# Kernel tuning notes

Hardware: AMD Instinct MI355X
Metric: run time of the kernel (lower is better)

## Reference

```python
import jax, jax.numpy as jnp
import numpy as np

N = 8192
E = 262144
D = 512

def _glorot(key, shape):
    fan_in, fan_out = shape[0], shape[1]
    lim = np.sqrt(6.0 / (fan_in + fan_out)).astype(np.float32)
    return jax.random.uniform(key, shape, jnp.float32, -lim, lim)

def setup_inputs() -> dict:
    key = jax.random.key(0)
    ks = jax.random.split(key, 16)
    x = jax.random.normal(ks[0], (N, D), jnp.float32)
    edge_index = jax.random.randint(ks[1], (2, E), 0, N, jnp.int64)
    return {
        "x": x,
        "edge_index": edge_index,
        # SAGEConv: lin_l applied to aggregated neighbors (has bias), lin_r to root
        "W_l": _glorot(ks[2], (D, D)), "b_l": jnp.zeros((D,), jnp.float32),
        "W_r": _glorot(ks[3], (D, D)),
        "Wa": _glorot(ks[4], (D, 256)), "ba": jnp.zeros((256,), jnp.float32),
        "W1": _glorot(ks[5], (256, 128)), "b1": jnp.zeros((128,), jnp.float32),
        "W2": _glorot(ks[6], (128, 64)), "b2": jnp.zeros((64,), jnp.float32),
        "W3": _glorot(ks[7], (64, 3)), "b3": jnp.zeros((3,), jnp.float32),
    }

def _sage_mean(x, edge_index):
    # message from src -> dst, mean aggregation over incoming edges
    src, dst = edge_index[0], edge_index[1]
    msg_sum = jax.ops.segment_sum(x[src], dst, num_segments=N)  # [N, D]
    deg = jax.ops.segment_sum(jnp.ones((edge_index.shape[1],), x.dtype), dst, num_segments=N)
    return msg_sum / jnp.maximum(deg, 1.0)[:, None]

def _cdist(y):
    # pairwise euclidean distances, stable sqrt (0 on the diagonal)
    sq = jnp.sum(y * y, axis=-1)
    d2 = sq[:, None] + sq[None, :] - 2.0 * (y @ y.T)
    d2 = jnp.maximum(d2, 0.0)
    safe = jnp.where(d2 > 0.0, d2, 1.0)
    return jnp.where(d2 > 0.0, jnp.sqrt(safe), 0.0)

def reference(x, edge_index, W_l, b_l, W_r, Wa, ba, W1, b1, W2, b2, W3, b3):
    agg = _sage_mean(x, edge_index)
    h = agg @ W_l + b_l + x @ W_r          # SAGEConv output [N, 512]
    h = jax.nn.relu(h)
    h = jax.nn.relu(h @ Wa + ba)           # [N, 256]
    h = jax.nn.relu(h @ W1 + b1)           # [N, 128]
    h = jax.nn.relu(h @ W2 + b2)           # [N, 64]
    h = h @ W3 + b3                        # [N, 3]
    return _cdist(h)                       # [N, N]
```

## Files before the change

### kernel.cpp

```cpp
#include <hip/hip_runtime.h>
#include <math.h>

#define NN 8192
#define DD 512
#define HB 64
#define PAD 128

typedef _Float16 f16;
typedef _Float16 half8 __attribute__((ext_vector_type(8)));
typedef _Float16 half4 __attribute__((ext_vector_type(4)));
typedef float f32x4 __attribute__((ext_vector_type(4)));

typedef const __attribute__((address_space(1))) unsigned int* gptr_t;
typedef __attribute__((address_space(3))) unsigned int* lptr_t;

__device__ __forceinline__ void gload16(const void* g, void* l) {
    __builtin_amdgcn_global_load_lds((gptr_t)g, (lptr_t)l, 16, 0, 0);
}

__device__ __forceinline__ void transpose_tile(const float* __restrict__ W,
                                               f16* __restrict__ Wt,
                                               int Kw, int Nw, int bx, int by,
                                               float (*tile)[33]) {
    int n0 = bx * 32, k0 = by * 32;
    int t = threadIdx.x;
    {
        int r = t >> 3, cq = (t & 7) * 4;
        float4 v = *(const float4*)(W + (size_t)(k0 + r) * Nw + n0 + cq);
        tile[r][cq] = v.x; tile[r][cq + 1] = v.y; tile[r][cq + 2] = v.z; tile[r][cq + 3] = v.w;
    }
    __syncthreads();
    {
        int n = t >> 3, rq = (t & 7) * 4;
        half4 h;
        h[0] = (f16)tile[rq][n];     h[1] = (f16)tile[rq + 1][n];
        h[2] = (f16)tile[rq + 2][n]; h[3] = (f16)tile[rq + 3][n];
        *(half4*)(Wt + (size_t)(n0 + n) * Kw + k0 + rq) = h;
    }
}

__global__ __launch_bounds__(256) void prep_hist(const float* __restrict__ x,
                                                 f16* __restrict__ xh,
                                                 const float* __restrict__ W_l, f16* __restrict__ Wlt,
                                                 const float* __restrict__ W_r, f16* __restrict__ Wrt,
                                                 const float* __restrict__ Wa,  f16* __restrict__ Wat,
                                                 const float* __restrict__ W1,  f16* __restrict__ W1t,
                                                 const int* __restrict__ ei,
                                                 int* __restrict__ locoff, int E) {
    __shared__ float tile[32][33];
    __shared__ int h[NN];
    int b = blockIdx.x;
    int t = threadIdx.x;
    if (b < 4096) {
        int i = b * 256 + t;
        float4 v = ((const float4*)x)[i];
        half4 hh;
        hh[0] = (f16)v.x; hh[1] = (f16)v.y; hh[2] = (f16)v.z; hh[3] = (f16)v.w;
        ((half4*)xh)[i] = hh;
        return;
    }
    b -= 4096;
    if (b < 256)      { transpose_tile(W_l, Wlt, 512, 512, b & 15, b >> 4, tile); return; }
    b -= 256;
    if (b < 256)      { transpose_tile(W_r, Wrt, 512, 512, b & 15, b >> 4, tile); return; }
    b -= 256;
    if (b < 128)      { transpose_tile(Wa, Wat, 512, 256, b & 7, b >> 3, tile); return; }
    b -= 128;
    if (b < 32)       { transpose_tile(W1, W1t, 256, 128, b & 3, b >> 2, tile); return; }
    b -= 32;
#pragma unroll
    for (int i = 0; i < NN / 256; i++) h[i * 256 + t] = 0;
    __syncthreads();
    int epb = (E + HB - 1) / HB;
    int e0 = b * epb, e1 = min(e0 + epb, E);
    for (int e = e0 + t; e < e1; e += 256)
        atomicAdd(&h[ei[E + e]], 1);
    __syncthreads();
#pragma unroll
    for (int i = 0; i < NN / 256; i++) {
        int n = i * 256 + t;
        locoff[(size_t)b * NN + n] = h[n];
    }
}

__global__ __launch_bounds__(256) void offs_kernel(int* __restrict__ locoff,
                                                   int* __restrict__ deg) {
    int n = blockIdx.x * 256 + threadIdx.x;
    int s = 0;
#pragma unroll 8
    for (int b = 0; b < HB; b++) {
        int v = locoff[(size_t)b * NN + n];
        locoff[(size_t)b * NN + n] = s;
        s += v;
    }
    deg[n] = s;
}

__global__ __launch_bounds__(256) void scatter_kernel(const int* __restrict__ ei,
                                                      const int* __restrict__ locoff,
                                                      int* __restrict__ csr_pad, int E) {
    __shared__ int cur[NN];
    int b = blockIdx.x, t = threadIdx.x;
#pragma unroll
    for (int i = 0; i < NN / 256; i++) {
        int n = i * 256 + t;
        cur[n] = locoff[(size_t)b * NN + n];
    }
    __syncthreads();
    int epb = (E + HB - 1) / HB;
    int e0 = b * epb, e1 = min(e0 + epb, E);
    for (int e = e0 + t; e < e1; e += 256) {
        int dst = ei[E + e];
        int src = ei[e];
        int slot = atomicAdd(&cur[dst], 1);
        if (slot < PAD)
            csr_pad[((size_t)dst << 7) + slot] = src;
    }
}

__global__ __launch_bounds__(256) void agg_kernel(const f16* __restrict__ xh,
                                                  const int* __restrict__ deg,
                                                  const int* __restrict__ csr_pad,
                                                  f16* __restrict__ aggh) {
    int node = blockIdx.x * 4 + (threadIdx.x >> 6);
    int l = threadIdx.x & 63;
    int e = deg[node];
    if (e > PAD) e = PAD;
    const int* lst = csr_pad + (node << 7);
    const half8* xb = (const half8*)xh;
    float acc[8] = {0, 0, 0, 0, 0, 0, 0, 0};
    int p = 0;
    for (; p + 4 <= e; p += 4) {
        int s0 = lst[p], s1 = lst[p + 1], s2 = lst[p + 2], s3 = lst[p + 3];
        half8 v0 = xb[(size_t)s0 * 64 + l];
        half8 v1 = xb[(size_t)s1 * 64 + l];
        half8 v2 = xb[(size_t)s2 * 64 + l];
        half8 v3 = xb[(size_t)s3 * 64 + l];
#pragma unroll
        for (int j = 0; j < 8; j++)
            acc[j] += (float)v0[j] + (float)v1[j] + (float)v2[j] + (float)v3[j];
    }
    for (; p < e; p++) {
        half8 v = xb[(size_t)lst[p] * 64 + l];
#pragma unroll
        for (int j = 0; j < 8; j++) acc[j] += (float)v[j];
    }
    float inv = 1.0f / fmaxf((float)deg[node], 1.0f);
    half8 h;
#pragma unroll
    for (int j = 0; j < 8; j++) h[j] = (f16)(acc[j] * inv);
    ((half8*)aggh)[(size_t)node * 64 + l] = h;
}

template<int BN>
__global__ __launch_bounds__(256) void gemm_thin(const f16* __restrict__ A1,
                                                 const f16* __restrict__ B1,
                                                 const f16* __restrict__ A2,
                                                 const f16* __restrict__ B2,
                                                 const float* __restrict__ bias,
                                                 f16* __restrict__ C,
                                                 int N, int K, int relu) {
    constexpr int BM = 32;
    constexpr int FM = 2;
    constexpr int FN = BN / 64;
    constexpr int ACH = BM / 16;
    constexpr int NCH = (BM + BN) / 16;
    __shared__ f16 As[2][BM * 32];
    __shared__ f16 Bs[2][BN * 32];

    const int tid = threadIdx.x;
    const int l = tid & 63;
    const int wid = tid >> 6;
    const int row0 = blockIdx.y * BM;
    const int col0 = blockIdx.x * BN;
    const int rowc = l >> 2;
    const int sp = l & 3;

    f32x4 acc[FM][FN];
#pragma unroll
    for (int i = 0; i < FM; i++)
#pragma unroll
        for (int j = 0; j < FN; j++)
#pragma unroll
            for (int q = 0; q < 4; q++) acc[i][j][q] = 0.0f;

    const int ktiles = K >> 5;
    const int npass = (A2 != nullptr) ? 2 : 1;
    const int nt = ktiles * npass;

    auto stage = [&](int buf, int t) {
        int pass = (t >= ktiles) ? 1 : 0;
        int kk = (t - pass * ktiles) << 5;
        const f16* Ag = pass ? A2 : A1;
        const f16* Bg = pass ? B2 : B1;
#pragma unroll
        for (int c = wid; c < NCH; c += 4) {
            bool isA = (c < ACH);
            int cc = isA ? c : c - ACH;
            int row = cc * 16 + rowc;
            int slot = sp ^ ((row >> 1) & 3);
            const f16* g;
            f16* ld;
            if (isA) {
                g = Ag + (size_t)(row0 + row) * K + kk + slot * 8;
                ld = &As[buf][cc * 512];
            } else {
                g = Bg + (size_t)(col0 + row) * K + kk + slot * 8;
                ld = &Bs[buf][cc * 512];
            }
            gload16(g, ld);
        }
    };

    stage(0, 0);
    __syncthreads();
    for (int t = 0; t < nt; ++t) {
        int cur = t & 1;
        if (t + 1 < nt) stage(cur ^ 1, t + 1);
        half8 af[FM], bf[FN];
#pragma unroll
        for (int i = 0; i < FM; i++) {
            int r = i * 16 + (l & 15);
            int off = r * 64 + ((((l >> 4) ^ ((r >> 1) & 3))) << 4);
            af[i] = *(const half8*)((const char*)As[cur] + off);
        }
#pragma unroll
        for (int j = 0; j < FN; j++) {
            int r = wid * FN * 16 + j * 16 + (l & 15);
            int off = r * 64 + ((((l >> 4) ^ ((r >> 1) & 3))) << 4);
            bf[j] = *(const half8*)((const char*)Bs[cur] + off);
        }
#pragma unroll
        for (int i = 0; i < FM; i++)
#pragma unroll
            for (int j = 0; j < FN; j++)
                acc[i][j] = __builtin_amdgcn_mfma_f32_16x16x32_f16(af[i], bf[j], acc[i][j], 0, 0, 0);
        __syncthreads();
    }

#pragma unroll
    for (int i = 0; i < FM; i++)
#pragma unroll
        for (int j = 0; j < FN; j++) {
            int row = row0 + i * 16 + ((l >> 4) << 2);
            int col = col0 + wid * FN * 16 + j * 16 + (l & 15);
            float bv = bias[col];
#pragma unroll
            for (int q = 0; q < 4; q++) {
                float v = acc[i][j][q] + bv;
                if (relu) v = fmaxf(v, 0.0f);
                C[(size_t)(row + q) * N + col] = (f16)v;
            }
        }
}

__global__ __launch_bounds__(256) void mlp_tail(const f16* __restrict__ h1,
                                                const f16* __restrict__ Wat,
                                                const float* __restrict__ ba,
                                                const f16* __restrict__ W1t,
                                                const float* __restrict__ b1,
                                                const float* __restrict__ W2,
                                                const float* __restrict__ b2,
                                                const float* __restrict__ W3,
                                                const float* __restrict__ b3,
                                                float* __restrict__ yv) {
    __shared__ f16 As2[2][32 * 32];
    __shared__ f16 Bs2[2][256 * 32];
    __shared__ f16 Bs3[2][128 * 32];
    __shared__ f16 h2s[32][264];
    __shared__ f16 h3s[32][136];

    const int tidx = threadIdx.x;
    const int l = tidx & 63;
    const int wid = tidx >> 6;
    const int row0 = blockIdx.x * 32;
    const int rowc = l >> 2;
    const int sp = l & 3;

    f32x4 acc2[2][4];
#pragma unroll
    for (int i = 0; i < 2; i++)
#pragma unroll
        for (int j = 0; j < 4; j++)
#pragma unroll
            for (int q = 0; q < 4; q++) acc2[i][j][q] = 0.0f;

    auto stage2 = [&](int buf, int t) {
        int kk = t << 5;
#pragma unroll
        for (int c = wid; c < 18; c += 4) {
            bool isA = (c < 2);
            int cc = isA ? c : c - 2;
            int row = cc * 16 + rowc;
            int slot = sp ^ ((row >> 1) & 3);
            if (isA) gload16(h1 + (size_t)(row0 + row) * 512 + kk + slot * 8, &As2[buf][cc * 512]);
            else     gload16(Wat + (size_t)row * 512 + kk + slot * 8, &Bs2[buf][cc * 512]);
        }
    };
    stage2(0, 0);
    __syncthreads();
    for (int t = 0; t < 16; ++t) {
        int cur = t & 1;
        if (t + 1 < 16) stage2(cur ^ 1, t + 1);
        half8 af[2], bf[4];
#pragma unroll
        for (int i = 0; i < 2; i++) {
            int r = i * 16 + (l & 15);
            int off = r * 64 + ((((l >> 4) ^ ((r >> 1) & 3))) << 4);
            af[i] = *(const half8*)((const char*)As2[cur] + off);
        }
#pragma unroll
        for (int j = 0; j < 4; j++) {
            int r = wid * 64 + j * 16 + (l & 15);
            int off = r * 64 + ((((l >> 4) ^ ((r >> 1) & 3))) << 4);
            bf[j] = *(const half8*)((const char*)Bs2[cur] + off);
        }
#pragma unroll
        for (int i = 0; i < 2; i++)
#pragma unroll
            for (int j = 0; j < 4; j++)
                acc2[i][j] = __builtin_amdgcn_mfma_f32_16x16x32_f16(af[i], bf[j], acc2[i][j], 0, 0, 0);
        __syncthreads();
    }
#pragma unroll
    for (int i = 0; i < 2; i++)
#pragma unroll
        for (int j = 0; j < 4; j++) {
            int rl = i * 16 + ((l >> 4) << 2);
            int cl = wid * 64 + j * 16 + (l & 15);
            float bv = ba[cl];
#pragma unroll
            for (int q = 0; q < 4; q++)
                h2s[rl + q][cl] = (f16)fmaxf(acc2[i][j][q] + bv, 0.0f);
        }

    f32x4 acc3[2][2];
#pragma unroll
    for (int i = 0; i < 2; i++)
#pragma unroll
        for (int j = 0; j < 2; j++)
#pragma unroll
            for (int q = 0; q < 4; q++) acc3[i][j][q] = 0.0f;

    auto stage3 = [&](int buf, int t) {
        int kk = t << 5;
#pragma unroll
        for (int c = wid; c < 8; c += 4) {
            int row = c * 16 + rowc;
            int slot = sp ^ ((row >> 1) & 3);
            gload16(W1t + (size_t)row * 256 + kk + slot * 8, &Bs3[buf][c * 512]);
        }
    };
    stage3(0, 0);
    __syncthreads();
    for (int t = 0; t < 8; ++t) {
        int cur = t & 1;
        if (t + 1 < 8) stage3(cur ^ 1, t + 1);
        half8 af[2], bf[2];
#pragma unroll
        for (int i = 0; i < 2; i++)
            af[i] = *(const half8*)&h2s[(l & 15) + 16 * i][t * 32 + (l >> 4) * 8];
#pragma unroll
        for (int j = 0; j < 2; j++) {
            int r = wid * 32 + j * 16 + (l & 15);
            int off = r * 64 + ((((l >> 4) ^ ((r >> 1) & 3))) << 4);
            bf[j] = *(const half8*)((const char*)Bs3[cur] + off);
        }
#pragma unroll
        for (int i = 0; i < 2; i++)
#pragma unroll
            for (int j = 0; j < 2; j++)
                acc3[i][j] = __builtin_amdgcn_mfma_f32_16x16x32_f16(af[i], bf[j], acc3[i][j], 0, 0, 0);
        __syncthreads();
    }
#pragma unroll
    for (int i = 0; i < 2; i++)
#pragma unroll
        for (int j = 0; j < 2; j++) {
            int rl = i * 16 + ((l >> 4) << 2);
            int cl = wid * 32 + j * 16 + (l & 15);
            float bv = b1[cl];
#pragma unroll
            for (int q = 0; q < 4; q++)
                h3s[rl + q][cl] = (f16)fmaxf(acc3[i][j][q] + bv, 0.0f);
        }
    __syncthreads();

    int row = tidx >> 3;
    int p = tidx & 7;
    int c0 = p * 8;
    float a8[8];
#pragma unroll
    for (int c = 0; c < 8; c++) a8[c] = b2[c0 + c];
    for (int k = 0; k < 128; k++) {
        float v = (float)h3s[row][k];
        const float4* w = (const float4*)(W2 + (size_t)k * 64 + c0);
        float4 w0 = w[0], w1 = w[1];
        a8[0] += v * w0.x; a8[1] += v * w0.y; a8[2] += v * w0.z; a8[3] += v * w0.w;
        a8[4] += v * w1.x; a8[5] += v * w1.y; a8[6] += v * w1.z; a8[7] += v * w1.w;
    }
    float a0 = 0.f, a1 = 0.f, a2 = 0.f;
#pragma unroll
    for (int c = 0; c < 8; c++) {
        float h = fmaxf(a8[c], 0.0f);
        int k = c0 + c;
        a0 += h * W3[k * 3 + 0];
        a1 += h * W3[k * 3 + 1];
        a2 += h * W3[k * 3 + 2];
    }
    a0 += __shfl_xor(a0, 1); a1 += __shfl_xor(a1, 1); a2 += __shfl_xor(a2, 1);
    a0 += __shfl_xor(a0, 2); a1 += __shfl_xor(a1, 2); a2 += __shfl_xor(a2, 2);
    a0 += __shfl_xor(a0, 4); a1 += __shfl_xor(a1, 4); a2 += __shfl_xor(a2, 4);
    if (p == 0)
        ((float4*)yv)[row0 + row] = make_float4(a0 + b3[0], a1 + b3[1], a2 + b3[2], 0.0f);
}

__global__ __launch_bounds__(256) void cdist_kernel(const float* __restrict__ y4,
                                                    float* __restrict__ out) {
    int tx = threadIdx.x & 63;
    int ty = threadIdx.x >> 6;
    int j0 = blockIdx.x * 256 + tx * 4;
    int i0 = blockIdx.y * 64 + ty * 16;
    const float4* yv = (const float4*)y4;
    float jx[4], jy[4], jz[4];
#pragma unroll
    for (int j = 0; j < 4; j++) {
        float4 t = yv[j0 + j];
        jx[j] = t.x; jy[j] = t.y; jz[j] = t.z;
    }
#pragma unroll
    for (int i = 0; i < 16; i++) {
        float4 ti = yv[i0 + i];
        f32x4 o;
#pragma unroll
        for (int j = 0; j < 4; j++) {
            float dx = ti.x - jx[j];
            float dy = ti.y - jy[j];
            float dz = ti.z - jz[j];
            o[j] = sqrtf(dx * dx + dy * dy + dz * dz);
        }
        __builtin_nontemporal_store(o, (f32x4*)(out + (size_t)(i0 + i) * NN + j0));
    }
}

extern "C" void kernel_launch(void* const* d_in, const int* in_sizes, int n_in,
                              void* d_out, int out_size, void* d_ws, size_t ws_size,
                              hipStream_t stream) {
    const float* x   = (const float*)d_in[0];
    const int*   ei  = (const int*)d_in[1];
    const float* W_l = (const float*)d_in[2];
    const float* b_l = (const float*)d_in[3];
    const float* W_r = (const float*)d_in[4];
    const float* Wa  = (const float*)d_in[5];
    const float* ba  = (const float*)d_in[6];
    const float* W1  = (const float*)d_in[7];
    const float* b1  = (const float*)d_in[8];
    const float* W2  = (const float*)d_in[9];
    const float* b2  = (const float*)d_in[10];
    const float* W3  = (const float*)d_in[11];
    const float* b3  = (const float*)d_in[12];
    float* out = (float*)d_out;
    const int E = in_sizes[1] / 2;

    auto al = [](size_t b) { return (b + 255) & ~(size_t)255; };
    const size_t small_need = al(NN * 4) +
                              al((size_t)NN * PAD * 4) +
                              al((size_t)HB * NN * 4) +
                              al((size_t)NN * 16) +
                              al(512 * 512 * 2) * 2 + al(512 * 256 * 2) +
                              al(256 * 128 * 2);
    const size_t act_need = al((size_t)NN * 512 * 2) * 3;
    char* sbase;
    char* abase;
    if (ws_size >= small_need + act_need) {
        sbase = (char*)d_ws; abase = (char*)d_ws + small_need;
    } else if (ws_size >= small_need) {
        sbase = (char*)d_ws; abase = (char*)d_out;
    } else {
        sbase = (char*)d_out; abase = (char*)d_out + small_need;
    }
    size_t so = 0, ao = 0;
    auto carve_s = [&](size_t b) { char* p = sbase + so; so += al(b); return p; };
    auto carve_a = [&](size_t b) { char* p = abase + ao; ao += al(b); return p; };

    int*   deg     = (int*)carve_s(NN * 4);
    int*   csr_pad = (int*)carve_s((size_t)NN * PAD * 4);
    int*   locoff  = (int*)carve_s((size_t)HB * NN * 4);
    float* yv      = (float*)carve_s((size_t)NN * 16);
    f16*   Wlt     = (f16*)carve_s(512 * 512 * 2);
    f16*   Wrt     = (f16*)carve_s(512 * 512 * 2);
    f16*   Wat     = (f16*)carve_s(512 * 256 * 2);
    f16*   W1t     = (f16*)carve_s(256 * 128 * 2);

    f16* x_h   = (f16*)carve_a((size_t)NN * 512 * 2);
    f16* agg_h = (f16*)carve_a((size_t)NN * 512 * 2);
    f16* h1    = (f16*)carve_a((size_t)NN * 512 * 2);

    prep_hist<<<4096 + 256 + 256 + 128 + 32 + HB, 256, 0, stream>>>(
        x, x_h, W_l, Wlt, W_r, Wrt, Wa, Wat, W1, W1t, ei, locoff, E);

    offs_kernel<<<NN / 256, 256, 0, stream>>>(locoff, deg);

    scatter_kernel<<<HB, 256, 0, stream>>>(ei, locoff, csr_pad, E);

    agg_kernel<<<NN / 4, 256, 0, stream>>>(x_h, deg, csr_pad, agg_h);

    gemm_thin<256><<<dim3(2, 256), 256, 0, stream>>>(
        agg_h, Wlt, x_h, Wrt, b_l, h1, 512, 512, 1);

    mlp_tail<<<NN / 32, 256, 0, stream>>>(h1, Wat, ba, W1t, b1, W2, b2, W3, b3, yv);

    cdist_kernel<<<dim3(NN / 256, NN / 64), 256, 0, stream>>>(yv, out);
}
```

Baseline: 161.0 us.

## Fuse SAGE GEMM into MLP tail kernel and merge offset scan into scatter

The SAGEConv dual GEMM (agg@W_l + x@W_r) is folded into the MLP kernel, so each 32-row block computes its full 512-wide h1 tile in shared memory instead of writing h1 to global and reading it back. The separate offset-scan kernel is removed; each scatter block now computes its own prefix over the per-block histograms, and the last block writes the degrees. This saves two launches and an 8 MB round trip of h1. In exchange each block uses much more LDS (a 64 KB B pool plus h1 tile), which lowers occupancy, and the GEMM grid shrinks from 512 to 256 blocks, each with a larger accumulator tile.

```diff
diff --git a/kernel.cpp b/kernel.cpp
--- a/kernel.cpp
+++ b/kernel.cpp
@@ -83,28 +83,25 @@
     }
 }
 
-__global__ __launch_bounds__(256) void offs_kernel(int* __restrict__ locoff,
-                                                   int* __restrict__ deg) {
-    int n = blockIdx.x * 256 + threadIdx.x;
-    int s = 0;
-#pragma unroll 8
-    for (int b = 0; b < HB; b++) {
-        int v = locoff[(size_t)b * NN + n];
-        locoff[(size_t)b * NN + n] = s;
-        s += v;
-    }
-    deg[n] = s;
-}
-
-__global__ __launch_bounds__(256) void scatter_kernel(const int* __restrict__ ei,
-                                                      const int* __restrict__ locoff,
-                                                      int* __restrict__ csr_pad, int E) {
+__global__ __launch_bounds__(256) void scatter_offs(const int* __restrict__ ei,
+                                                    const int* __restrict__ locoff,
+                                                    int* __restrict__ deg,
+                                                    int* __restrict__ csr_pad, int E) {
     __shared__ int cur[NN];
     int b = blockIdx.x, t = threadIdx.x;
 #pragma unroll
     for (int i = 0; i < NN / 256; i++) {
         int n = i * 256 + t;
-        cur[n] = locoff[(size_t)b * NN + n];
+        int s = 0;
+        int bb = 0;
+        for (; bb + 4 <= b; bb += 4)
+            s += locoff[(size_t)bb * NN + n] + locoff[(size_t)(bb + 1) * NN + n] +
+                 locoff[(size_t)(bb + 2) * NN + n] + locoff[(size_t)(bb + 3) * NN + n];
+        for (; bb < b; bb++)
+            s += locoff[(size_t)bb * NN + n];
+        cur[n] = s;
+        if (b == HB - 1)
+            deg[n] = s + locoff[(size_t)b * NN + n];
     }
     __syncthreads();
     int epb = (E + HB - 1) / HB;
@@ -152,123 +149,26 @@
     ((half8*)aggh)[(size_t)node * 64 + l] = h;
 }
 
-template<int BN>
-__global__ __launch_bounds__(256) void gemm_thin(const f16* __restrict__ A1,
-                                                 const f16* __restrict__ B1,
-                                                 const f16* __restrict__ A2,
-                                                 const f16* __restrict__ B2,
-                                                 const float* __restrict__ bias,
-                                                 f16* __restrict__ C,
-                                                 int N, int K, int relu) {
-    constexpr int BM = 32;
-    constexpr int FM = 2;
-    constexpr int FN = BN / 64;
-    constexpr int ACH = BM / 16;
-    constexpr int NCH = (BM + BN) / 16;
-    __shared__ f16 As[2][BM * 32];
-    __shared__ f16 Bs[2][BN * 32];
-
-    const int tid = threadIdx.x;
-    const int l = tid & 63;
-    const int wid = tid >> 6;
-    const int row0 = blockIdx.y * BM;
-    const int col0 = blockIdx.x * BN;
-    const int rowc = l >> 2;
-    const int sp = l & 3;
-
-    f32x4 acc[FM][FN];
-#pragma unroll
-    for (int i = 0; i < FM; i++)
-#pragma unroll
-        for (int j = 0; j < FN; j++)
-#pragma unroll
-            for (int q = 0; q < 4; q++) acc[i][j][q] = 0.0f;
-
-    const int ktiles = K >> 5;
-    const int npass = (A2 != nullptr) ? 2 : 1;
-    const int nt = ktiles * npass;
-
-    auto stage = [&](int buf, int t) {
-        int pass = (t >= ktiles) ? 1 : 0;
-        int kk = (t - pass * ktiles) << 5;
-        const f16* Ag = pass ? A2 : A1;
-        const f16* Bg = pass ? B2 : B1;
-#pragma unroll
-        for (int c = wid; c < NCH; c += 4) {
-            bool isA = (c < ACH);
-            int cc = isA ? c : c - ACH;
-            int row = cc * 16 + rowc;
-            int slot = sp ^ ((row >> 1) & 3);
-            const f16* g;
-            f16* ld;
-            if (isA) {
-                g = Ag + (size_t)(row0 + row) * K + kk + slot * 8;
-                ld = &As[buf][cc * 512];
-            } else {
-                g = Bg + (size_t)(col0 + row) * K + kk + slot * 8;
-                ld = &Bs[buf][cc * 512];
-            }
-            gload16(g, ld);
-        }
-    };
-
-    stage(0, 0);
-    __syncthreads();
-    for (int t = 0; t < nt; ++t) {
-        int cur = t & 1;
-        if (t + 1 < nt) stage(cur ^ 1, t + 1);
-        half8 af[FM], bf[FN];
-#pragma unroll
-        for (int i = 0; i < FM; i++) {
-            int r = i * 16 + (l & 15);
-            int off = r * 64 + ((((l >> 4) ^ ((r >> 1) & 3))) << 4);
-            af[i] = *(const half8*)((const char*)As[cur] + off);
-        }
-#pragma unroll
-        for (int j = 0; j < FN; j++) {
-            int r = wid * FN * 16 + j * 16 + (l & 15);
-            int off = r * 64 + ((((l >> 4) ^ ((r >> 1) & 3))) << 4);
-            bf[j] = *(const half8*)((const char*)Bs[cur] + off);
-        }
-#pragma unroll
-        for (int i = 0; i < FM; i++)
-#pragma unroll
-            for (int j = 0; j < FN; j++)
-                acc[i][j] = __builtin_amdgcn_mfma_f32_16x16x32_f16(af[i], bf[j], acc[i][j], 0, 0, 0);
-        __syncthreads();
-    }
-
-#pragma unroll
-    for (int i = 0; i < FM; i++)
-#pragma unroll
-        for (int j = 0; j < FN; j++) {
-            int row = row0 + i * 16 + ((l >> 4) << 2);
-            int col = col0 + wid * FN * 16 + j * 16 + (l & 15);
-            float bv = bias[col];
-#pragma unroll
-            for (int q = 0; q < 4; q++) {
-                float v = acc[i][j][q] + bv;
-                if (relu) v = fmaxf(v, 0.0f);
-                C[(size_t)(row + q) * N + col] = (f16)v;
-            }
-        }
-}
-
-__global__ __launch_bounds__(256) void mlp_tail(const f16* __restrict__ h1,
-                                                const f16* __restrict__ Wat,
-                                                const float* __restrict__ ba,
-                                                const f16* __restrict__ W1t,
-                                                const float* __restrict__ b1,
-                                                const float* __restrict__ W2,
-                                                const float* __restrict__ b2,
-                                                const float* __restrict__ W3,
-                                                const float* __restrict__ b3,
-                                                float* __restrict__ yv) {
-    __shared__ f16 As2[2][32 * 32];
-    __shared__ f16 Bs2[2][256 * 32];
-    __shared__ f16 Bs3[2][128 * 32];
+__global__ __launch_bounds__(256) void mlp_all(const f16* __restrict__ agg_h,
+                                               const f16* __restrict__ x_h,
+                                               const f16* __restrict__ Wlt,
+                                               const f16* __restrict__ Wrt,
+                                               const float* __restrict__ b_l,
+                                               const f16* __restrict__ Wat,
+                                               const float* __restrict__ ba,
+                                               const f16* __restrict__ W1t,
+                                               const float* __restrict__ b1,
+                                               const float* __restrict__ W2,
+                                               const float* __restrict__ b2,
+                                               const float* __restrict__ W3,
+                                               const float* __restrict__ b3,
+                                               float* __restrict__ yv) {
+    __shared__ f16 BsPool[2 * 16384];
+    __shared__ f16 As[2][1024];
+    __shared__ f16 h1s[32][516];
     __shared__ f16 h2s[32][264];
     __shared__ f16 h3s[32][136];
+    char* Bs0 = (char*)BsPool;
 
     const int tidx = threadIdx.x;
     const int l = tidx & 63;
@@ -277,142 +177,206 @@
     const int rowc = l >> 2;
     const int sp = l & 3;
 
-    f32x4 acc2[2][4];
-#pragma unroll
-    for (int i = 0; i < 2; i++)
-#pragma unroll
-        for (int j = 0; j < 4; j++)
-#pragma unroll
-            for (int q = 0; q < 4; q++) acc2[i][j][q] = 0.0f;
-
-    auto stage2 = [&](int buf, int t) {
-        int kk = t << 5;
-#pragma unroll
-        for (int c = wid; c < 18; c += 4) {
-            bool isA = (c < 2);
-            int cc = isA ? c : c - 2;
-            int row = cc * 16 + rowc;
-            int slot = sp ^ ((row >> 1) & 3);
-            if (isA) gload16(h1 + (size_t)(row0 + row) * 512 + kk + slot * 8, &As2[buf][cc * 512]);
-            else     gload16(Wat + (size_t)row * 512 + kk + slot * 8, &Bs2[buf][cc * 512]);
-        }
-    };
-    stage2(0, 0);
-    __syncthreads();
-    for (int t = 0; t < 16; ++t) {
-        int cur = t & 1;
-        if (t + 1 < 16) stage2(cur ^ 1, t + 1);
-        half8 af[2], bf[4];
-#pragma unroll
-        for (int i = 0; i < 2; i++) {
-            int r = i * 16 + (l & 15);
-            int off = r * 64 + ((((l >> 4) ^ ((r >> 1) & 3))) << 4);
-            af[i] = *(const half8*)((const char*)As2[cur] + off);
-        }
-#pragma unroll
-        for (int j = 0; j < 4; j++) {
-            int r = wid * 64 + j * 16 + (l & 15);
-            int off = r * 64 + ((((l >> 4) ^ ((r >> 1) & 3))) << 4);
-            bf[j] = *(const half8*)((const char*)Bs2[cur] + off);
-        }
+    {
+        f32x4 acc[2][8];
+#pragma unroll
+        for (int i = 0; i < 2; i++)
+#pragma unroll
+            for (int j = 0; j < 8; j++)
+#pragma unroll
+                for (int q = 0; q < 4; q++) acc[i][j][q] = 0.0f;
+
+        auto stage = [&](int buf, int t) {
+            int pass = t >> 4;
+            int kk = (t & 15) << 5;
+            const f16* Ag = pass ? x_h : agg_h;
+            const f16* Bg = pass ? Wrt : Wlt;
+            for (int c = wid; c < 34; c += 4) {
+                bool isA = (c < 2);
+                int cc = isA ? c : c - 2;
+                int row = cc * 16 + rowc;
+                int slot = sp ^ ((row >> 1) & 3);
+                if (isA) gload16(Ag + (size_t)(row0 + row) * 512 + kk + slot * 8,
+                                 &As[buf][cc * 512]);
+                else     gload16(Bg + (size_t)row * 512 + kk + slot * 8,
+                                 (f16*)(Bs0 + (size_t)buf * 32768) + cc * 512);
+            }
+        };
+        stage(0, 0);
+        __syncthreads();
+        for (int t = 0; t < 32; ++t) {
+            int cur = t & 1;
+            if (t + 1 < 32) stage(cur ^ 1, t + 1);
+            half8 af[2], bf[8];
+#pragma unroll
+            for (int i = 0; i < 2; i++) {
+                int r = i * 16 + (l & 15);
+                int off = r * 64 + ((((l >> 4) ^ ((r >> 1) & 3))) << 4);
+                af[i] = *(const half8*)((const char*)As[cur] + off);
+            }
+#pragma unroll
+            for (int j = 0; j < 8; j++) {
+                int r = wid * 128 + j * 16 + (l & 15);
+                int off = r * 64 + ((((l >> 4) ^ ((r >> 1) & 3))) << 4);
+                bf[j] = *(const half8*)(Bs0 + (size_t)cur * 32768 + off);
+            }
+#pragma unroll
+            for (int i = 0; i < 2; i++)
+#pragma unroll
+                for (int j = 0; j < 8; j++)
+                    acc[i][j] = __builtin_amdgcn_mfma_f32_16x16x32_f16(af[i], bf[j], acc[i][j], 0, 0, 0);
+            __syncthreads();
+        }
+#pragma unroll
+        for (int i = 0; i < 2; i++)
+#pragma unroll
+            for (int j = 0; j < 8; j++) {
+                int rl = i * 16 + ((l >> 4) << 2);
+                int cl = wid * 128 + j * 16 + (l & 15);
+                float bv = b_l[cl];
+#pragma unroll
+                for (int q = 0; q < 4; q++)
+                    h1s[rl + q][cl] = (f16)fmaxf(acc[i][j][q] + bv, 0.0f);
+            }
+    }
+    __syncthreads();
+
+    {
+        f32x4 acc2[2][4];
 #pragma unroll
         for (int i = 0; i < 2; i++)
 #pragma unroll
             for (int j = 0; j < 4; j++)
-                acc2[i][j] = __builtin_amdgcn_mfma_f32_16x16x32_f16(af[i], bf[j], acc2[i][j], 0, 0, 0);
+#pragma unroll
+                for (int q = 0; q < 4; q++) acc2[i][j][q] = 0.0f;
+
+        auto stage2 = [&](int buf, int t) {
+            int kk = t << 5;
+            for (int c = wid; c < 16; c += 4) {
+                int row = c * 16 + rowc;
+                int slot = sp ^ ((row >> 1) & 3);
+                gload16(Wat + (size_t)row * 512 + kk + slot * 8,
+                        (f16*)(Bs0 + (size_t)buf * 16384) + c * 512);
+            }
+        };
+        stage2(0, 0);
         __syncthreads();
-    }
-#pragma unroll
-    for (int i = 0; i < 2; i++)
-#pragma unroll
-        for (int j = 0; j < 4; j++) {
-            int rl = i * 16 + ((l >> 4) << 2);
-            int cl = wid * 64 + j * 16 + (l & 15);
-            float bv = ba[cl];
-#pragma unroll
-            for (int q = 0; q < 4; q++)
-                h2s[rl + q][cl] = (f16)fmaxf(acc2[i][j][q] + bv, 0.0f);
-        }
-
-    f32x4 acc3[2][2];
-#pragma unroll
-    for (int i = 0; i < 2; i++)
-#pragma unroll
-        for (int j = 0; j < 2; j++)
-#pragma unroll
-            for (int q = 0; q < 4; q++) acc3[i][j][q] = 0.0f;
-
-    auto stage3 = [&](int buf, int t) {
-        int kk = t << 5;
-#pragma unroll
-        for (int c = wid; c < 8; c += 4) {
-            int row = c * 16 + rowc;
-            int slot = sp ^ ((row >> 1) & 3);
-            gload16(W1t + (size_t)row * 256 + kk + slot * 8, &Bs3[buf][c * 512]);
-        }
-    };
-    stage3(0, 0);
-    __syncthreads();
-    for (int t = 0; t < 8; ++t) {
-        int cur = t & 1;
-        if (t + 1 < 8) stage3(cur ^ 1, t + 1);
-        half8 af[2], bf[2];
-#pragma unroll
-        for (int i = 0; i < 2; i++)
-            af[i] = *(const half8*)&h2s[(l & 15) + 16 * i][t * 32 + (l >> 4) * 8];
-#pragma unroll
-        for (int j = 0; j < 2; j++) {
-            int r = wid * 32 + j * 16 + (l & 15);
-            int off = r * 64 + ((((l >> 4) ^ ((r >> 1) & 3))) << 4);
-            bf[j] = *(const half8*)((const char*)Bs3[cur] + off);
-        }
+        for (int t = 0; t < 16; ++t) {
+            int cur = t & 1;
+            if (t + 1 < 16) stage2(cur ^ 1, t + 1);
+            half8 af[2], bf[4];
+#pragma unroll
+            for (int i = 0; i < 2; i++)
+                af[i] = *(const half8*)&h1s[(l & 15) + 16 * i][t * 32 + (l >> 4) * 8];
+#pragma unroll
+            for (int j = 0; j < 4; j++) {
+                int r = wid * 64 + j * 16 + (l & 15);
+                int off = r * 64 + ((((l >> 4) ^ ((r >> 1) & 3))) << 4);
+                bf[j] = *(const half8*)(Bs0 + (size_t)cur * 16384 + off);
+            }
+#pragma unroll
+            for (int i = 0; i < 2; i++)
+#pragma unroll
+                for (int j = 0; j < 4; j++)
+                    acc2[i][j] = __builtin_amdgcn_mfma_f32_16x16x32_f16(af[i], bf[j], acc2[i][j], 0, 0, 0);
+            __syncthreads();
+        }
+#pragma unroll
+        for (int i = 0; i < 2; i++)
+#pragma unroll
+            for (int j = 0; j < 4; j++) {
+                int rl = i * 16 + ((l >> 4) << 2);
+                int cl = wid * 64 + j * 16 + (l & 15);
+                float bv = ba[cl];
+#pragma unroll
+                for (int q = 0; q < 4; q++)
+                    h2s[rl + q][cl] = (f16)fmaxf(acc2[i][j][q] + bv, 0.0f);
+            }
+    }
+
+    {
+        f32x4 acc3[2][2];
 #pragma unroll
         for (int i = 0; i < 2; i++)
 #pragma unroll
             for (int j = 0; j < 2; j++)
-                acc3[i][j] = __builtin_amdgcn_mfma_f32_16x16x32_f16(af[i], bf[j], acc3[i][j], 0, 0, 0);
+#pragma unroll
+                for (int q = 0; q < 4; q++) acc3[i][j][q] = 0.0f;
+
+        auto stage3 = [&](int buf, int t) {
+            int kk = t << 5;
+            for (int c = wid; c < 8; c += 4) {
+                int row = c * 16 + rowc;
+                int slot = sp ^ ((row >> 1) & 3);
+                gload16(W1t + (size_t)row * 256 + kk + slot * 8,
+                        (f16*)(Bs0 + (size_t)buf * 8192) + c * 512);
+            }
+        };
+        stage3(0, 0);
         __syncthreads();
-    }
-#pragma unroll
-    for (int i = 0; i < 2; i++)
-#pragma unroll
-        for (int j = 0; j < 2; j++) {
-            int rl = i * 16 + ((l >> 4) << 2);
-            int cl = wid * 32 + j * 16 + (l & 15);
-            float bv = b1[cl];
-#pragma unroll
-            for (int q = 0; q < 4; q++)
-                h3s[rl + q][cl] = (f16)fmaxf(acc3[i][j][q] + bv, 0.0f);
-        }
-    __syncthreads();
-
-    int row = tidx >> 3;
-    int p = tidx & 7;
-    int c0 = p * 8;
-    float a8[8];
-#pragma unroll
-    for (int c = 0; c < 8; c++) a8[c] = b2[c0 + c];
-    for (int k = 0; k < 128; k++) {
-        float v = (float)h3s[row][k];
-        const float4* w = (const float4*)(W2 + (size_t)k * 64 + c0);
-        float4 w0 = w[0], w1 = w[1];
-        a8[0] += v * w0.x; a8[1] += v * w0.y; a8[2] += v * w0.z; a8[3] += v * w0.w;
-        a8[4] += v * w1.x; a8[5] += v * w1.y; a8[6] += v * w1.z; a8[7] += v * w1.w;
-    }
-    float a0 = 0.f, a1 = 0.f, a2 = 0.f;
-#pragma unroll
-    for (int c = 0; c < 8; c++) {
-        float h = fmaxf(a8[c], 0.0f);
-        int k = c0 + c;
-        a0 += h * W3[k * 3 + 0];
-        a1 += h * W3[k * 3 + 1];
-        a2 += h * W3[k * 3 + 2];
-    }
-    a0 += __shfl_xor(a0, 1); a1 += __shfl_xor(a1, 1); a2 += __shfl_xor(a2, 1);
-    a0 += __shfl_xor(a0, 2); a1 += __shfl_xor(a1, 2); a2 += __shfl_xor(a2, 2);
-    a0 += __shfl_xor(a0, 4); a1 += __shfl_xor(a1, 4); a2 += __shfl_xor(a2, 4);
-    if (p == 0)
-        ((float4*)yv)[row0 + row] = make_float4(a0 + b3[0], a1 + b3[1], a2 + b3[2], 0.0f);
+        for (int t = 0; t < 8; ++t) {
+            int cur = t & 1;
+            if (t + 1 < 8) stage3(cur ^ 1, t + 1);
+            half8 af[2], bf[2];
+#pragma unroll
+            for (int i = 0; i < 2; i++)
+                af[i] = *(const half8*)&h2s[(l & 15) + 16 * i][t * 32 + (l >> 4) * 8];
+#pragma unroll
+            for (int j = 0; j < 2; j++) {
+                int r = wid * 32 + j * 16 + (l & 15);
+                int off = r * 64 + ((((l >> 4) ^ ((r >> 1) & 3))) << 4);
+                bf[j] = *(const half8*)(Bs0 + (size_t)cur * 8192 + off);
+            }
+#pragma unroll
+            for (int i = 0; i < 2; i++)
+#pragma unroll
+                for (int j = 0; j < 2; j++)
+                    acc3[i][j] = __builtin_amdgcn_mfma_f32_16x16x32_f16(af[i], bf[j], acc3[i][j], 0, 0, 0);
+            __syncthreads();
+        }
+#pragma unroll
+        for (int i = 0; i < 2; i++)
+#pragma unroll
+            for (int j = 0; j < 2; j++) {
+                int rl = i * 16 + ((l >> 4) << 2);
+                int cl = wid * 32 + j * 16 + (l & 15);
+                float bv = b1[cl];
+#pragma unroll
+                for (int q = 0; q < 4; q++)
+                    h3s[rl + q][cl] = (f16)fmaxf(acc3[i][j][q] + bv, 0.0f);
+            }
+    }
+    __syncthreads();
+
+    {
+        int row = tidx >> 3;
+        int p = tidx & 7;
+        int c0 = p * 8;
+        float a8[8];
+#pragma unroll
+        for (int c = 0; c < 8; c++) a8[c] = b2[c0 + c];
+        for (int k = 0; k < 128; k++) {
+            float v = (float)h3s[row][k];
+            const float4* w = (const float4*)(W2 + (size_t)k * 64 + c0);
+            float4 w0 = w[0], w1 = w[1];
+            a8[0] += v * w0.x; a8[1] += v * w0.y; a8[2] += v * w0.z; a8[3] += v * w0.w;
+            a8[4] += v * w1.x; a8[5] += v * w1.y; a8[6] += v * w1.z; a8[7] += v * w1.w;
+        }
+        float a0 = 0.f, a1 = 0.f, a2 = 0.f;
+#pragma unroll
+        for (int c = 0; c < 8; c++) {
+            float h = fmaxf(a8[c], 0.0f);
+            int k = c0 + c;
+            a0 += h * W3[k * 3 + 0];
+            a1 += h * W3[k * 3 + 1];
+            a2 += h * W3[k * 3 + 2];
+        }
+        a0 += __shfl_xor(a0, 1); a1 += __shfl_xor(a1, 1); a2 += __shfl_xor(a2, 1);
+        a0 += __shfl_xor(a0, 2); a1 += __shfl_xor(a1, 2); a2 += __shfl_xor(a2, 2);
+        a0 += __shfl_xor(a0, 4); a1 += __shfl_xor(a1, 4); a2 += __shfl_xor(a2, 4);
+        if (p == 0)
+            ((float4*)yv)[row0 + row] = make_float4(a0 + b3[0], a1 + b3[1], a2 + b3[2], 0.0f);
+    }
 }
 
 __global__ __launch_bounds__(256) void cdist_kernel(const float* __restrict__ y4,
@@ -469,7 +433,7 @@
                               al((size_t)NN * 16) +
                               al(512 * 512 * 2) * 2 + al(512 * 256 * 2) +
                               al(256 * 128 * 2);
-    const size_t act_need = al((size_t)NN * 512 * 2) * 3;
+    const size_t act_need = al((size_t)NN * 512 * 2) * 2;
     char* sbase;
     char* abase;
     if (ws_size >= small_need + act_need) {
@@ -494,21 +458,16 @@
 
     f16* x_h   = (f16*)carve_a((size_t)NN * 512 * 2);
     f16* agg_h = (f16*)carve_a((size_t)NN * 512 * 2);
-    f16* h1    = (f16*)carve_a((size_t)NN * 512 * 2);
 
     prep_hist<<<4096 + 256 + 256 + 128 + 32 + HB, 256, 0, stream>>>(
         x, x_h, W_l, Wlt, W_r, Wrt, Wa, Wat, W1, W1t, ei, locoff, E);
 
-    offs_kernel<<<NN / 256, 256, 0, stream>>>(locoff, deg);
-
-    scatter_kernel<<<HB, 256, 0, stream>>>(ei, locoff, csr_pad, E);
+    scatter_offs<<<HB, 256, 0, stream>>>(ei, locoff, deg, csr_pad, E);
 
     agg_kernel<<<NN / 4, 256, 0, stream>>>(x_h, deg, csr_pad, agg_h);
 
-    gemm_thin<256><<<dim3(2, 256), 256, 0, stream>>>(
-        agg_h, Wlt, x_h, Wrt, b_l, h1, 512, 512, 1);
-
-    mlp_tail<<<NN / 32, 256, 0, stream>>>(h1, Wat, ba, W1t, b1, W2, b2, W3, b3, yv);
+    mlp_all<<<NN / 32, 256, 0, stream>>>(agg_h, x_h, Wlt, Wrt, b_l,
+                                         Wat, ba, W1t, b1, W2, b2, W3, b3, yv);
 
     cdist_kernel<<<dim3(NN / 256, NN / 64), 256, 0, stream>>>(yv, out);
 }
```

Measured after the change: 249.2 us. 54.8% more time.
